# Optimization experiments

Measured on AMD Instinct MI355X. Metric: run time of the kernel, lower is better.

The kernel has to match this reference:

```python
import jax, jax.numpy as jnp
import numpy as np

D_MODEL = 1024
N_HEADS = 16
MAX_LEN = 2048
B, T = 4, 2048


def _rope_tables(max_len, head_dim):
    # freqs = 1 / 10000^(arange(0,d,2)/d); angles = outer(pos, freqs)
    freqs = 1.0 / (10000.0 ** (jnp.arange(0, head_dim, 2, dtype=jnp.float32) / head_dim))
    angles = jnp.arange(max_len, dtype=jnp.float32)[:, None] * freqs[None, :]  # [max_len, d/2]
    return jnp.cos(angles), jnp.sin(angles)


def _rope(x, cos, sin):
    # x: [B, H, T, d], interleaved rotate: pairs (x[...,0::2], x[...,1::2])
    t = x.shape[2]
    c = cos[:t][None, None]  # [1,1,T,d/2]
    s = sin[:t][None, None]
    x1, x2 = x[..., 0::2], x[..., 1::2]
    out = jnp.stack([x1 * c - x2 * s, x1 * s + x2 * c], axis=-1)  # [B,H,T,d/2,2]
    return out.reshape(x.shape)


def setup_inputs() -> dict:
    key = jax.random.key(0)
    kx, kq, kk, kv, ko = jax.random.split(key, 5)
    scale = 1.0 / np.sqrt(D_MODEL)
    return {
        "x": jax.random.normal(kx, (B, T, D_MODEL), dtype=jnp.float32),
        "Wq": jax.random.normal(kq, (D_MODEL, D_MODEL), dtype=jnp.float32) * scale,
        "Wk": jax.random.normal(kk, (D_MODEL, D_MODEL), dtype=jnp.float32) * scale,
        "Wv": jax.random.normal(kv, (D_MODEL, D_MODEL), dtype=jnp.float32) * scale,
        "Wo": jax.random.normal(ko, (D_MODEL, D_MODEL), dtype=jnp.float32) * scale,
    }


def reference(x, Wq, Wk, Wv, Wo):
    b, t, d_model = x.shape
    h = N_HEADS
    d = d_model // h
    cos, sin = _rope_tables(MAX_LEN, d)

    # nn.Linear(bias=False): y = x @ W.T
    def proj(W):
        return (x @ W.T).reshape(b, t, h, d).transpose(0, 2, 1, 3)  # [B,H,T,d]

    q = _rope(proj(Wq), cos, sin)
    k = _rope(proj(Wk), cos, sin)
    v = proj(Wv)

    scale = 1.0 / jnp.sqrt(jnp.asarray(d, dtype=x.dtype))
    scores = jnp.einsum("bhqd,bhkd->bhqk", q, k) * scale  # [B,H,T,T]
    causal = jnp.tril(jnp.ones((t, t), dtype=bool))
    scores = jnp.where(causal[None, None], scores, jnp.finfo(x.dtype).min)
    attn = jax.nn.softmax(scores, axis=-1)
    ctx = jnp.einsum("bhqk,bhkd->bhqd", attn, v)  # [B,H,T,d]
    ctx = ctx.transpose(0, 2, 1, 3).reshape(b, t, d_model)
    return ctx @ Wo.T
```

## Files before the change

### kernel.cpp

```cpp
#include <hip/hip_runtime.h>
#include <hip/hip_bf16.h>
#include <stdint.h>
#include <math.h>

#define D_MODEL 1024
#define NH 16
#define HD 64
#define BATCH 4
#define SEQ 2048
#define MTOT (BATCH*SEQ)
#define NBH (BATCH*NH)

typedef __attribute__((ext_vector_type(8))) short short8;
typedef __attribute__((ext_vector_type(4))) short short4v;
typedef __attribute__((ext_vector_type(2))) unsigned uint2v;
typedef __attribute__((ext_vector_type(4))) unsigned uint4v;
typedef __attribute__((ext_vector_type(4))) float f32x4;
typedef __attribute__((ext_vector_type(16))) float f32x16;

static __device__ __forceinline__ unsigned short f2bf(float f) {
  union { float f; unsigned u; } v; v.f = f;
  unsigned r = v.u + 0x7FFFu + ((v.u >> 16) & 1u);
  return (unsigned short)(r >> 16);
}

static __device__ __forceinline__ unsigned cvt_pk_bf16(float lo, float hi) {
  unsigned r;
  asm("v_cvt_pk_bf16_f32 %0, %1, %2" : "=v"(r) : "v"(lo), "v"(hi));
  return r;
}

static __device__ __forceinline__ float fexp2(float x) {
#if __has_builtin(__builtin_amdgcn_exp2f)
  return __builtin_amdgcn_exp2f(x);
#else
  return __expf(x * 0.69314718056f);
#endif
}

#define GLOAD16(g, l) __builtin_amdgcn_global_load_lds( \
    (const __attribute__((address_space(1))) unsigned int*)(g), \
    (__attribute__((address_space(3))) unsigned int*)(l), 16, 0, 0)

__global__ __launch_bounds__(256) void k_prep(
    const float* __restrict__ x, const float* __restrict__ wq,
    const float* __restrict__ wk, const float* __restrict__ wv,
    const float* __restrict__ wo,
    unsigned short* __restrict__ xb, unsigned short* __restrict__ wb,
    float* __restrict__ cosT, float* __restrict__ sinT) {
  long i = (long)blockIdx.x * 256 + threadIdx.x;
  const long NX = (long)MTOT * D_MODEL;
  const long NW = (long)D_MODEL * D_MODEL;
  if (i < NX) { xb[i] = f2bf(x[i]); return; }
  i -= NX;
  if (i < NW) { wb[i] = f2bf(wq[i]); return; }
  i -= NW;
  if (i < NW) { wb[NW + i] = f2bf(wk[i]); return; }
  i -= NW;
  if (i < NW) { wb[2 * NW + i] = f2bf(wv[i]); return; }
  i -= NW;
  if (i < NW) { wb[3 * NW + i] = f2bf(wo[i]); return; }
  i -= NW;
  if (i < (long)SEQ * (HD / 2)) {
    int t = (int)(i & (SEQ - 1)), j = (int)(i >> 11);
    float freq = 1.0f / powf(10000.0f, (float)j * (1.0f / 32.0f));
    float ang = (float)t * freq;
    cosT[j * SEQ + t] = cosf(ang);
    sinT[j * SEQ + t] = sinf(ang);
  }
}

template<int EPI>
__global__ __launch_bounds__(256) void k_gemm(
    const unsigned short* __restrict__ A, const unsigned short* __restrict__ Bw,
    unsigned short* __restrict__ q, unsigned short* __restrict__ k2,
    unsigned short* __restrict__ vt,
    const float* __restrict__ cosT, const float* __restrict__ sinT,
    float* __restrict__ outf) {
  __shared__ __align__(16) unsigned short As[128 * 32];
  __shared__ __align__(16) unsigned short Bs[128 * 32];
  const int tid = threadIdx.x;
  const int wid = tid >> 6, lane = tid & 63;
  const int l15 = lane & 15, lq = lane >> 4;
  const int m0 = blockIdx.x * 128, n0 = blockIdx.y * 128;
  const int wm = (wid >> 1) * 64, wn = (wid & 1) * 64;

  const f32x4 fz = {0.f, 0.f, 0.f, 0.f};
  f32x4 acc[4][4];
#pragma unroll
  for (int i = 0; i < 4; ++i)
#pragma unroll
    for (int j = 0; j < 4; ++j) acc[i][j] = fz;

  const int srow = wid * 16 + (lane >> 2);
  const int scol = (lane & 3) * 8;
  const unsigned short* Ag = A + (long)(m0 + srow) * D_MODEL + scol;
  const unsigned short* Bg = Bw + (long)(n0 + srow) * D_MODEL + scol;

  for (int k0 = 0; k0 < D_MODEL; k0 += 32) {
    GLOAD16(Ag + k0, As + wid * 512);
    GLOAD16(Ag + k0 + 64 * D_MODEL, As + 2048 + wid * 512);
    GLOAD16(Bg + k0, Bs + wid * 512);
    GLOAD16(Bg + k0 + 64 * D_MODEL, Bs + 2048 + wid * 512);
    __syncthreads();

    short8 af[4], bf[4];
#pragma unroll
    for (int i = 0; i < 4; ++i) {
      af[i] = *(const short8*)(As + (wm + i * 16 + l15) * 32 + lq * 8);
      bf[i] = *(const short8*)(Bs + (wn + i * 16 + l15) * 32 + lq * 8);
    }
#pragma unroll
    for (int i = 0; i < 4; ++i)
#pragma unroll
      for (int j = 0; j < 4; ++j)
        acc[i][j] = __builtin_amdgcn_mfma_f32_16x16x32_bf16(af[i], bf[j], acc[i][j], 0, 0, 0);
    __syncthreads();
  }

#pragma unroll
  for (int i = 0; i < 4; ++i) {
#pragma unroll
    for (int j = 0; j < 4; ++j) {
      if (EPI == 1) {
#pragma unroll
        for (int r = 0; r < 4; ++r) {
          const int m = m0 + wm + i * 16 + lq * 4 + r;
          const int n = n0 + wn + j * 16 + l15;
          outf[(long)m * D_MODEL + n] = acc[i][j][r];
        }
      } else {
        const int n = n0 + wn + j * 16 + l15;
        const int sel = n >> 10, nl = n & 1023;
        const int hh = nl >> 6, dd = nl & 63;
        const int mb = m0 + wm + i * 16 + lq * 4;
        const int bb = mb >> 11, t0 = mb & (SEQ - 1);
        const long bh = (long)bb * NH + hh;
        if (sel == 2) {
          uint2v pk;
          pk[0] = cvt_pk_bf16(acc[i][j][0], acc[i][j][1]);
          pk[1] = cvt_pk_bf16(acc[i][j][2], acc[i][j][3]);
          *(uint2v*)(vt + (bh * HD + dd) * SEQ + t0) = pk;
        } else {
          unsigned short* dst = (sel == 0) ? q : k2;
          const float qs = (sel == 0) ? 0.18033688011112793f : 1.0f;
          const float sgn = (dd & 1) ? 1.f : -1.f;
          const int jt = dd >> 1;
          const f32x4 cv = *(const f32x4*)(cosT + jt * SEQ + t0);
          const f32x4 sv = *(const f32x4*)(sinT + jt * SEQ + t0);
#pragma unroll
          for (int r = 0; r < 4; ++r) {
            const float val = acc[i][j][r];
            const float p = __shfl_xor(val, 1);
            dst[((bh * SEQ + t0 + r) << 6) + dd] = f2bf((val * cv[r] + sgn * sv[r] * p) * qs);
          }
        }
      }
    }
  }
}

__global__ __launch_bounds__(256, 3) void k_attn(
    const unsigned short* __restrict__ qb, const unsigned short* __restrict__ kb,
    const unsigned short* __restrict__ vt, unsigned short* __restrict__ ctx) {
  __shared__ __align__(16) unsigned short Ks[2][4096];
  __shared__ __align__(16) unsigned short Vs[2][4096];

  const int orig = blockIdx.x;
  const int c = orig & 255, rr = orig >> 8;
  const int x = c & 7, y = c >> 3;
  const int u = y & 3, g = y >> 2;
  const int bh = x * 8 + g;
  const int blk = (rr & 1) ? (15 - ((rr >> 1) << 2) - u)
                           : (u + ((rr >> 1) << 2));
  const int ntB = 2 * blk + 2;

  const int tid = threadIdx.x;
  const int wid = tid >> 6, lane = tid & 63;
  const int l31 = lane & 31, hi = lane >> 5;
  const int qrow0w = blk * 128 + wid * 32;
  const int qg = qrow0w + l31;

  const unsigned short* Kg = kb + ((long)bh * SEQ << 6);
  const unsigned short* Vg = vt + (long)bh * HD * SEQ;

  const int r0 = tid >> 3, c0 = tid & 7;
  const int r1 = r0 + 32;
  const int cs = c0 ^ (r0 & 7);

  const unsigned short* Qrow = qb + (((long)bh * SEQ + qrow0w + l31) << 6);
  short8 bq[4];
#pragma unroll
  for (int kbI = 0; kbI < 4; ++kbI)
    bq[kbI] = *(const short8*)(Qrow + kbI * 16 + hi * 8);

  f32x16 ota[2];
#pragma unroll
  for (int a2 = 0; a2 < 2; ++a2)
#pragma unroll
    for (int r = 0; r < 16; ++r) ota[a2][r] = 0.f;
  float m = -INFINITY, lsum = 0.f;

#define STAGE(t_) { \
    const long kv0s = (long)((t_) << 6); \
    unsigned short* kd = Ks[(t_) & 1]; \
    unsigned short* vd = Vs[(t_) & 1]; \
    GLOAD16(Kg + ((kv0s + r0) << 6) + (cs << 3), kd + wid * 512); \
    GLOAD16(Kg + ((kv0s + r1) << 6) + (cs << 3), kd + 2048 + wid * 512); \
    GLOAD16(Vg + (long)r0 * SEQ + kv0s + (cs << 3), vd + wid * 512); \
    GLOAD16(Vg + (long)r1 * SEQ + kv0s + (cs << 3), vd + 2048 + wid * 512); \
  }

  STAGE(0);

  for (int t = 0; t < ntB; ++t) {
    const int kv0 = t << 6;
    if (t + 1 < ntB) {
      STAGE(t + 1);
      asm volatile("s_waitcnt vmcnt(4)" ::: "memory");
    } else {
      asm volatile("s_waitcnt vmcnt(0)" ::: "memory");
    }
    __builtin_amdgcn_s_barrier();

    if (kv0 <= qrow0w + 31) {
      const char* Kb = (const char*)Ks[t & 1];
      const char* Vb = (const char*)Vs[t & 1];

      f32x16 sa[2];
#pragma unroll
      for (int i = 0; i < 2; ++i)
#pragma unroll
        for (int r = 0; r < 16; ++r) sa[i][r] = 0.f;

      __builtin_amdgcn_s_setprio(1);
#pragma unroll
      for (int i = 0; i < 2; ++i) {
        const int row = 32 * i + l31;
        const int rb = row << 7, rx = row & 7;
#pragma unroll
        for (int kbI = 0; kbI < 4; ++kbI) {
          const short8 ak = *(const short8*)(Kb + rb + ((((kbI << 1) | hi) ^ rx) << 4));
          sa[i] = __builtin_amdgcn_mfma_f32_32x32x16_bf16(ak, bq[kbI], sa[i], 0, 0, 0);
        }
      }
      __builtin_amdgcn_s_setprio(0);

      if (kv0 + 63 > qrow0w) {
#pragma unroll
        for (int i = 0; i < 2; ++i) {
          const int kvb = kv0 + 32 * i + 4 * hi;
#pragma unroll
          for (int r = 0; r < 16; ++r)
            if (kvb + (r & 3) + 8 * (r >> 2) > qg) sa[i][r] = -INFINITY;
        }
      }

      float tmax = sa[0][0];
#pragma unroll
      for (int i = 0; i < 2; ++i)
#pragma unroll
        for (int r = 0; r < 16; ++r) tmax = fmaxf(tmax, sa[i][r]);
      tmax = fmaxf(tmax, __shfl_xor(tmax, 32));
      if (!__all(tmax <= m + 8.0f)) {
        const float mn = fmaxf(m, tmax);
        const float al = fexp2(m - mn);
        m = mn;
        lsum *= al;
#pragma unroll
        for (int a2 = 0; a2 < 2; ++a2)
#pragma unroll
          for (int r = 0; r < 16; ++r) ota[a2][r] *= al;
      }
      float rs = 0.f;
#pragma unroll
      for (int i = 0; i < 2; ++i)
#pragma unroll
        for (int r = 0; r < 16; ++r) {
          const float p = fexp2(sa[i][r] - m);
          sa[i][r] = p;
          rs += p;
        }
      rs += __shfl_xor(rs, 32);
      lsum += rs;

      short8 bp[4];
#pragma unroll
      for (int i = 0; i < 2; ++i)
#pragma unroll
        for (int jh = 0; jh < 2; ++jh) {
          const int bs = 8 * jh;
          const unsigned x0 = cvt_pk_bf16(sa[i][bs + 0], sa[i][bs + 1]);
          const unsigned y0 = cvt_pk_bf16(sa[i][bs + 4], sa[i][bs + 5]);
          const unsigned x1 = cvt_pk_bf16(sa[i][bs + 2], sa[i][bs + 3]);
          const unsigned y1 = cvt_pk_bf16(sa[i][bs + 6], sa[i][bs + 7]);
          const uint2v s0 = __builtin_amdgcn_permlane32_swap(x0, y0, false, false);
          const uint2v s1 = __builtin_amdgcn_permlane32_swap(x1, y1, false, false);
          union { uint4v u4; short8 s; } bb;
          bb.u4[0] = s0[0]; bb.u4[1] = s1[0]; bb.u4[2] = s0[1]; bb.u4[3] = s1[1];
          bp[2 * i + jh] = bb.s;
        }

      __builtin_amdgcn_s_setprio(1);
#pragma unroll
      for (int a2 = 0; a2 < 2; ++a2) {
        const int row = 32 * a2 + l31;
        const int rb = row << 7, rx = row & 7;
#pragma unroll
        for (int kf = 0; kf < 4; ++kf) {
          const short8 av = *(const short8*)(Vb + rb + ((((kf << 1) | hi) ^ rx) << 4));
          ota[a2] = __builtin_amdgcn_mfma_f32_32x32x16_bf16(av, bp[kf], ota[a2], 0, 0, 0);
        }
      }
      __builtin_amdgcn_s_setprio(0);
    }

    asm volatile("" ::: "memory");
    __builtin_amdgcn_s_barrier();
  }
#undef STAGE

  const int b = bh >> 4, h = bh & 15;
  unsigned short* cb = ctx + (((long)b * SEQ) << 10) + (h << 6);
  const float inv = 1.0f / lsum;
  const long trow = qg;
#pragma unroll
  for (int a2 = 0; a2 < 2; ++a2)
#pragma unroll
    for (int rb4 = 0; rb4 < 4; ++rb4) {
      const int d0 = 32 * a2 + 8 * rb4 + 4 * hi;
      uint2v pk;
      pk[0] = cvt_pk_bf16(ota[a2][4 * rb4 + 0] * inv, ota[a2][4 * rb4 + 1] * inv);
      pk[1] = cvt_pk_bf16(ota[a2][4 * rb4 + 2] * inv, ota[a2][4 * rb4 + 3] * inv);
      *(uint2v*)(cb + trow * D_MODEL + d0) = pk;
    }
}

extern "C" void kernel_launch(void* const* d_in, const int* in_sizes, int n_in,
                              void* d_out, int out_size, void* d_ws, size_t ws_size,
                              hipStream_t stream) {
  const float* x  = (const float*)d_in[0];
  const float* wq = (const float*)d_in[1];
  const float* wk = (const float*)d_in[2];
  const float* wv = (const float*)d_in[3];
  const float* wo = (const float*)d_in[4];
  float* out = (float*)d_out;
  char* ws = (char*)d_ws;

  unsigned short* xb  = (unsigned short*)(ws);
  unsigned short* wb  = (unsigned short*)(ws + (16l << 20));
  unsigned short* qb  = (unsigned short*)(ws + (24l << 20));
  unsigned short* kb  = (unsigned short*)(ws + (40l << 20));
  unsigned short* vt  = (unsigned short*)(ws + (56l << 20));
  float* cosT = (float*)(ws + (72l << 20));
  float* sinT = cosT + SEQ * 32;
  unsigned short* ctx = xb;

  const long ntot = (long)MTOT * D_MODEL + 4l * D_MODEL * D_MODEL + (long)SEQ * 32;
  k_prep<<<dim3((unsigned)((ntot + 255) / 256)), dim3(256), 0, stream>>>(
      x, wq, wk, wv, wo, xb, wb, cosT, sinT);
  k_gemm<0><<<dim3(64, 24), dim3(256), 0, stream>>>(
      xb, wb, qb, kb, vt, cosT, sinT, nullptr);
  k_attn<<<dim3(1024), dim3(256), 0, stream>>>(qb, kb, vt, ctx);
  k_gemm<1><<<dim3(64, 8), dim3(256), 0, stream>>>(
      ctx, wb + 3l * D_MODEL * D_MODEL, nullptr, nullptr, nullptr, nullptr, nullptr, out);
}
```

Before: 170.1 us.

## Double-buffer GEMM LDS tiles with BK=64, XOR swizzle, and phased prefetch

Rewrites the bf16 GEMM main loop to use two LDS buffers with a 64-wide K tile. Loads for the next tile are issued in stages between MFMA phases, with explicit vmcnt waits and barriers. LDS columns are XOR-swizzled to avoid bank conflicts, and MFMA phases are raised in priority with s_setprio. This aims to hide global-to-LDS latency and cut per-iteration sync overhead, at the cost of four times the LDS, which may lower occupancy, and fragile manual waitcnt ordering.

```diff
diff --git a/kernel.cpp b/kernel.cpp
--- a/kernel.cpp
+++ b/kernel.cpp
@@ -41,6 +41,9 @@
 #define GLOAD16(g, l) __builtin_amdgcn_global_load_lds( \
     (const __attribute__((address_space(1))) unsigned int*)(g), \
     (__attribute__((address_space(3))) unsigned int*)(l), 16, 0, 0)
+
+#define BAR() { asm volatile("" ::: "memory"); __builtin_amdgcn_s_barrier(); \
+                asm volatile("" ::: "memory"); }
 
 __global__ __launch_bounds__(256) void k_prep(
     const float* __restrict__ x, const float* __restrict__ wq,
@@ -70,6 +73,8 @@
   }
 }
 
+#define MFMA16(a, b, c) __builtin_amdgcn_mfma_f32_16x16x32_bf16(a, b, c, 0, 0, 0)
+
 template<int EPI>
 __global__ __launch_bounds__(256) void k_gemm(
     const unsigned short* __restrict__ A, const unsigned short* __restrict__ Bw,
@@ -77,8 +82,8 @@
     unsigned short* __restrict__ vt,
     const float* __restrict__ cosT, const float* __restrict__ sinT,
     float* __restrict__ outf) {
-  __shared__ __align__(16) unsigned short As[128 * 32];
-  __shared__ __align__(16) unsigned short Bs[128 * 32];
+  __shared__ __align__(16) unsigned short As2[2][128 * 64];
+  __shared__ __align__(16) unsigned short Bs2[2][128 * 64];
   const int tid = threadIdx.x;
   const int wid = tid >> 6, lane = tid & 63;
   const int l15 = lane & 15, lq = lane >> 4;
@@ -92,31 +97,79 @@
 #pragma unroll
     for (int j = 0; j < 4; ++j) acc[i][j] = fz;
 
-  const int srow = wid * 16 + (lane >> 2);
-  const int scol = (lane & 3) * 8;
-  const unsigned short* Ag = A + (long)(m0 + srow) * D_MODEL + scol;
-  const unsigned short* Bg = Bw + (long)(n0 + srow) * D_MODEL + scol;
-
-  for (int k0 = 0; k0 < D_MODEL; k0 += 32) {
-    GLOAD16(Ag + k0, As + wid * 512);
-    GLOAD16(Ag + k0 + 64 * D_MODEL, As + 2048 + wid * 512);
-    GLOAD16(Bg + k0, Bs + wid * 512);
-    GLOAD16(Bg + k0 + 64 * D_MODEL, Bs + 2048 + wid * 512);
-    __syncthreads();
-
-    short8 af[4], bf[4];
-#pragma unroll
-    for (int i = 0; i < 4; ++i) {
-      af[i] = *(const short8*)(As + (wm + i * 16 + l15) * 32 + lq * 8);
-      bf[i] = *(const short8*)(Bs + (wn + i * 16 + l15) * 32 + lq * 8);
+  const int sr = tid >> 3;
+  const int cs = (tid & 7) ^ (sr & 7);
+  const unsigned short* Ag = A + (long)(m0 + sr) * D_MODEL + cs * 8;
+  const unsigned short* Bg = Bw + (long)(n0 + sr) * D_MODEL + cs * 8;
+
+#define SA0(t_) { const long ko = (long)(t_) * 64; \
+    unsigned short* d = As2[(t_) & 1] + wid * 512; \
+    GLOAD16(Ag + ko, d); GLOAD16(Ag + ko + 32 * D_MODEL, d + 2048); }
+#define SA1(t_) { const long ko = (long)(t_) * 64; \
+    unsigned short* d = As2[(t_) & 1] + wid * 512; \
+    GLOAD16(Ag + ko + 64 * D_MODEL, d + 4096); \
+    GLOAD16(Ag + ko + 96 * D_MODEL, d + 6144); }
+#define SB0(t_) { const long ko = (long)(t_) * 64; \
+    unsigned short* d = Bs2[(t_) & 1] + wid * 512; \
+    GLOAD16(Bg + ko, d); GLOAD16(Bg + ko + 32 * D_MODEL, d + 2048); }
+#define SB1(t_) { const long ko = (long)(t_) * 64; \
+    unsigned short* d = Bs2[(t_) & 1] + wid * 512; \
+    GLOAD16(Bg + ko + 64 * D_MODEL, d + 4096); \
+    GLOAD16(Bg + ko + 96 * D_MODEL, d + 6144); }
+
+#define PHASE(I0, J0) do { \
+    const int ra0 = wm + (I0) * 16 + l15, ra1 = ra0 + 16; \
+    const int rx0 = ra0 & 7, rx1 = ra1 & 7; \
+    const short8 a00 = *(const short8*)(Ab + (ra0 << 7) + ((lq ^ rx0) << 4)); \
+    const short8 a01 = *(const short8*)(Ab + (ra0 << 7) + (((4 | lq) ^ rx0) << 4)); \
+    const short8 a10 = *(const short8*)(Ab + (ra1 << 7) + ((lq ^ rx1) << 4)); \
+    const short8 a11 = *(const short8*)(Ab + (ra1 << 7) + (((4 | lq) ^ rx1) << 4)); \
+    const int rb0 = wn + (J0) * 16 + l15, rb1 = rb0 + 16; \
+    const int sx0 = rb0 & 7, sx1 = rb1 & 7; \
+    const short8 b00 = *(const short8*)(Bb + (rb0 << 7) + ((lq ^ sx0) << 4)); \
+    const short8 b01 = *(const short8*)(Bb + (rb0 << 7) + (((4 | lq) ^ sx0) << 4)); \
+    const short8 b10 = *(const short8*)(Bb + (rb1 << 7) + ((lq ^ sx1) << 4)); \
+    const short8 b11 = *(const short8*)(Bb + (rb1 << 7) + (((4 | lq) ^ sx1) << 4)); \
+    __builtin_amdgcn_s_setprio(1); \
+    acc[(I0)][(J0)]         = MFMA16(a00, b00, acc[(I0)][(J0)]); \
+    acc[(I0)][(J0)]         = MFMA16(a01, b01, acc[(I0)][(J0)]); \
+    acc[(I0)][(J0) + 1]     = MFMA16(a00, b10, acc[(I0)][(J0) + 1]); \
+    acc[(I0)][(J0) + 1]     = MFMA16(a01, b11, acc[(I0)][(J0) + 1]); \
+    acc[(I0) + 1][(J0)]     = MFMA16(a10, b00, acc[(I0) + 1][(J0)]); \
+    acc[(I0) + 1][(J0)]     = MFMA16(a11, b01, acc[(I0) + 1][(J0)]); \
+    acc[(I0) + 1][(J0) + 1] = MFMA16(a10, b10, acc[(I0) + 1][(J0) + 1]); \
+    acc[(I0) + 1][(J0) + 1] = MFMA16(a11, b11, acc[(I0) + 1][(J0) + 1]); \
+    __builtin_amdgcn_s_setprio(0); \
+  } while (0)
+
+  SA0(0); SA1(0); SB0(0); SB1(0);
+  const int NT = D_MODEL / 64;
+  for (int t = 0; t < NT; ++t) {
+    const char* Ab = (const char*)As2[t & 1];
+    const char* Bb = (const char*)Bs2[t & 1];
+    if (t + 1 < NT) {
+      SA0(t + 1); SA1(t + 1);
+      asm volatile("s_waitcnt vmcnt(4)" ::: "memory");
+    } else {
+      asm volatile("s_waitcnt vmcnt(0)" ::: "memory");
     }
-#pragma unroll
-    for (int i = 0; i < 4; ++i)
-#pragma unroll
-      for (int j = 0; j < 4; ++j)
-        acc[i][j] = __builtin_amdgcn_mfma_f32_16x16x32_bf16(af[i], bf[j], acc[i][j], 0, 0, 0);
-    __syncthreads();
+    BAR();
+    PHASE(0, 0);
+    BAR();
+    if (t + 1 < NT) SB0(t + 1);
+    PHASE(2, 0);
+    BAR();
+    if (t + 1 < NT) SB1(t + 1);
+    PHASE(0, 2);
+    BAR();
+    PHASE(2, 2);
+    BAR();
   }
+#undef SA0
+#undef SA1
+#undef SB0
+#undef SB1
+#undef PHASE
 
 #pragma unroll
   for (int i = 0; i < 4; ++i) {
```

Result: slower. 208.6 us (+22.7%).
